# Kernel tuning notes

Measured on AMD Instinct MI355X. Metric: run time of the kernel, lower is better.

Reference implementation:

```python
import jax, jax.numpy as jnp
import numpy as np

N_ITER = 5  # from init_kwargs


def setup_inputs() -> dict:
    key = jax.random.key(0)
    k1, k2 = jax.random.split(key)
    K, F, B = 4, 513, 4000
    Xr = jax.random.normal(k1, (K, F, B), dtype=jnp.float32)
    Xi = jax.random.normal(k2, (K, F, B), dtype=jnp.float32)
    return {"Xr": Xr, "Xi": Xi}


def _auxiva(X):
    # X: complex64 (K, F, B)
    K, F, B = X.shape
    # XXh[i,j,f,b] = X[i,f,b] * conj(X[j,f,b])
    XXh = jnp.einsum('ifb,jfb->ijfb', X, X.conj())
    Wh = jnp.tile(jnp.eye(K, dtype=X.dtype)[None], (F, 1, 1))  # (F, K, K)
    for _ in range(N_ITER):
        Y = jnp.einsum('fsc,cfb->sfb', Wh, X)          # demix: (K, F, B)
        r = jnp.linalg.norm(Y, axis=1)                  # (K, B), real
        phi = 1.0 / (2.0 * r)                           # laplace contrast
        # V[k,i,j,f] = mean_b phi[k,b] * XXh[i,j,f,b]  (avoid (K,K,K,F,B) blowup)
        V = jnp.einsum('kb,ijfb->kijf', phi.astype(X.dtype), XXh) / B
        for k in range(K):                              # sequential IP updates
            M = jnp.einsum('fik,kjf->fij', Wh, V[k])    # (F, K, K)
            w = jnp.linalg.inv(M)[:, :, k].conj()       # (F, K)
            denom = jnp.sqrt(jnp.einsum('fc,ckf,fk->f', w, V[k], w.conj()))
            Wh = Wh.at[:, k, :].set(w / denom[:, None])
    Y = jnp.einsum('fsc,cfb->sfb', Wh, X)
    scale = jnp.linalg.inv(Wh)[:, :, 0]                 # projection back: (F, K)
    return jnp.einsum('sfb,fs->sfb', Y, scale)


def reference(Xr, Xi):
    X = (Xr + 1j * Xi).astype(jnp.complex64)
    return _auxiva(X)
```

## Files before the change

kernel.cpp:

```cpp
#include <hip/hip_runtime.h>
#include <hip/hip_bf16.h>
#include <math.h>

#define K 4
#define F 513
#define B 4000
#define NIT 5
#define FB (F*B)
#define KB (K*B)
#define DFC 4
#define NDF 129
#define NBC 8
#define BCH (B/NBC)

__device__ float2 g_Wh[F*16];
__device__ float2 g_Vp[NBC*64*F];
__device__ float2 g_scale[F*4];
__device__ float  g_r2p[NDF*KB];
__device__ float4 g_phiT[B];

struct cd { double re, im; };
__device__ inline cd mkcd(double r, double i){ cd z; z.re=r; z.im=i; return z; }
__device__ inline cd cmul(cd a, cd b){ return mkcd(a.re*b.re - a.im*b.im, a.re*b.im + a.im*b.re); }
__device__ inline cd cadd(cd a, cd b){ return mkcd(a.re+b.re, a.im+b.im); }
__device__ inline cd csub(cd a, cd b){ return mkcd(a.re-b.re, a.im-b.im); }
__device__ inline cd conj_(cd a){ return mkcd(a.re, -a.im); }
__device__ inline cd cdiv(cd a, cd b){
  double d = b.re*b.re + b.im*b.im;
  return mkcd((a.re*b.re + a.im*b.im)/d, (a.im*b.re - a.re*b.im)/d);
}

__device__ inline void invcol4(const cd M[4][4], int kk, cd x[4]){
  int r0 = (kk==0)?1:0;
  int r1 = (kk<=1)?2:1;
  int r2 = (kk<=2)?3:2;
  cd cof[4];
  #pragma unroll
  for (int i=0;i<4;++i){
    int c0 = (i==0)?1:0;
    int c1 = (i<=1)?2:1;
    int c2 = (i<=2)?3:2;
    cd m = cadd(csub(cmul(M[r0][c0], csub(cmul(M[r1][c1],M[r2][c2]), cmul(M[r1][c2],M[r2][c1]))),
                     cmul(M[r0][c1], csub(cmul(M[r1][c0],M[r2][c2]), cmul(M[r1][c2],M[r2][c0])))),
                cmul(M[r0][c2], csub(cmul(M[r1][c0],M[r2][c1]), cmul(M[r1][c1],M[r2][c0]))));
    if ((kk+i)&1) m = mkcd(-m.re,-m.im);
    cof[i] = m;
  }
  cd det = mkcd(0.0,0.0);
  #pragma unroll
  for (int i=0;i<4;++i) det = cadd(det, cmul(M[kk][i], cof[i]));
  cd idet = cdiv(mkcd(1.0,0.0), det);
  #pragma unroll
  for (int i=0;i<4;++i) x[i] = cmul(cof[i], idet);
}


__global__ void init_kernel(){
  int t = blockIdx.x*blockDim.x + threadIdx.x;
  if (t < F*16){
    int sc = t & 15; int s = sc >> 2, c = sc & 3;
    g_Wh[t] = make_float2(s==c ? 1.0f : 0.0f, 0.0f);
  }
}

__global__ __launch_bounds__(256) void demix_part_kernel(
    const float* __restrict__ Xr, const float* __restrict__ Xi){
  int t = blockIdx.x*blockDim.x + threadIdx.x;
  if (t >= B/2) return;
  int b = 2*t;
  int y = blockIdx.y;
  int f0 = y*DFC, f1 = min(f0+DFC, F);
  float acc0[K], acc1[K];
  #pragma unroll
  for (int s=0;s<K;++s){ acc0[s]=0.0f; acc1[s]=0.0f; }
  for (int f=f0; f<f1; ++f){
    float2 xr[K], xi[K];
    #pragma unroll
    for (int c=0;c<K;++c){
      int idx = c*FB + f*B + b;
      xr[c] = *reinterpret_cast<const float2*>(Xr + idx);
      xi[c] = *reinterpret_cast<const float2*>(Xi + idx);
    }
    const float2* w = g_Wh + f*16;
    #pragma unroll
    for (int s=0;s<K;++s){
      float yr0=0.0f, yi0=0.0f, yr1=0.0f, yi1=0.0f;
      #pragma unroll
      for (int c=0;c<K;++c){
        float2 ww = w[s*4+c];
        yr0 += ww.x*xr[c].x - ww.y*xi[c].x;
        yi0 += ww.x*xi[c].x + ww.y*xr[c].x;
        yr1 += ww.x*xr[c].y - ww.y*xi[c].y;
        yi1 += ww.x*xi[c].y + ww.y*xr[c].y;
      }
      acc0[s] += yr0*yr0 + yi0*yi0;
      acc1[s] += yr1*yr1 + yi1*yi1;
    }
  }
  #pragma unroll
  for (int s=0;s<K;++s)
    *reinterpret_cast<float2*>(g_r2p + y*KB + s*B + b) = make_float2(acc0[s], acc1[s]);
}

__global__ __launch_bounds__(256) void phi_kernel(){
  int b = blockIdx.x*blockDim.x + threadIdx.x;
  if (b >= B) return;
  int k = blockIdx.y;
  float s = 0.0f;
  #pragma unroll 8
  for (int y=0; y<NDF; ++y) s += g_r2p[y*KB + k*B + b];
  reinterpret_cast<float*>(g_phiT)[b*4 + k] = 0.5f / sqrtf(s);
}

__global__ __launch_bounds__(256, 4) void v_kernel(
    const float* __restrict__ Xr, const float* __restrict__ Xi){
  int f = blockIdx.x;
  int y = blockIdx.y;
  int tid = threadIdx.x;
  float acc[64];
  #pragma unroll
  for (int q=0;q<64;++q) acc[q]=0.0f;

  if (tid < BCH/2){
    int b = y*BCH + 2*tid;
    float4 ph0 = g_phiT[b];
    float4 ph1 = g_phiT[b+1];
    float pk0[K] = {ph0.x, ph0.y, ph0.z, ph0.w};
    float pk1[K] = {ph1.x, ph1.y, ph1.z, ph1.w};
    float2 xr[K], xi[K];
    #pragma unroll
    for (int c=0;c<K;++c){
      int idx = c*FB + f*B + b;
      xr[c] = *reinterpret_cast<const float2*>(Xr + idx);
      xi[c] = *reinterpret_cast<const float2*>(Xi + idx);
    }
    {
      float p[16];
      #pragma unroll
      for (int i=0;i<4;++i) p[i] = xr[i].x*xr[i].x + xi[i].x*xi[i].x;
      int s = 4;
      #pragma unroll
      for (int i=0;i<4;++i){
        #pragma unroll
        for (int j=i+1;j<4;++j){
          p[s++] = xr[i].x*xr[j].x + xi[i].x*xi[j].x;
          p[s++] = xi[i].x*xr[j].x - xr[i].x*xi[j].x;
        }
      }
      #pragma unroll
      for (int k=0;k<K;++k){
        #pragma unroll
        for (int q=0;q<16;++q) acc[k*16+q] += pk0[k]*p[q];
      }
    }
    {
      float p[16];
      #pragma unroll
      for (int i=0;i<4;++i) p[i] = xr[i].y*xr[i].y + xi[i].y*xi[i].y;
      int s = 4;
      #pragma unroll
      for (int i=0;i<4;++i){
        #pragma unroll
        for (int j=i+1;j<4;++j){
          p[s++] = xr[i].y*xr[j].y + xi[i].y*xi[j].y;
          p[s++] = xi[i].y*xr[j].y - xr[i].y*xi[j].y;
        }
      }
      #pragma unroll
      for (int k=0;k<K;++k){
        #pragma unroll
        for (int q=0;q<16;++q) acc[k*16+q] += pk1[k]*p[q];
      }
    }
  }

  int lane = tid & 63, wave = tid >> 6;
  #pragma unroll
  for (int d=0; d<6; ++d){
    const int sh = 1<<d;
    const bool hi = (lane & sh) != 0;
    #pragma unroll
    for (int m=0; m<(32>>d); ++m){
      float keep = hi ? acc[2*m+1] : acc[2*m];
      float send = hi ? acc[2*m]   : acc[2*m+1];
      acc[m] = keep + __shfl_xor(send, sh);
    }
  }

  __shared__ float part[4*64];
  __shared__ float red[64];
  part[wave*64 + lane] = acc[0];
  __syncthreads();
  if (tid < 64){
    red[tid] = (part[tid] + part[64+tid] + part[128+tid] + part[192+tid]) * (1.0f/B);
  }
  __syncthreads();
  if (tid < 64){
    int k = tid >> 4, ij = tid & 15, i = ij >> 2, j = ij & 3;
    float re, im;
    if (i == j){ re = red[k*16 + i]; im = 0.0f; }
    else {
      int a = min(i,j), c2 = max(i,j);
      int pidx = (a==0) ? (c2-1) : ((a==1) ? (c2+1) : 5);
      re = red[k*16 + 4 + 2*pidx];
      im = red[k*16 + 5 + 2*pidx];
      if (i > j) im = -im;
    }
    g_Vp[(y*64 + (unsigned)tid)*F + f] = make_float2(re, im);
  }
}

__global__ __launch_bounds__(64) void update_kernel(int do_scale){
  int f = blockIdx.x*blockDim.x + threadIdx.x;
  if (f >= F) return;
  cd W[4][4];
  #pragma unroll
  for (int s=0;s<4;++s)
    #pragma unroll
    for (int c=0;c<4;++c){ float2 w = g_Wh[f*16+s*4+c]; W[s][c] = mkcd((double)w.x,(double)w.y); }

  #pragma unroll
  for (int k=0;k<4;++k){
    cd Vk[4][4];
    #pragma unroll
    for (int i=0;i<4;++i)
      #pragma unroll
      for (int j=0;j<4;++j){
        float2 vv = make_float2(0.0f, 0.0f);
        #pragma unroll
        for (int y=0;y<NBC;++y){
          float2 t2 = g_Vp[(y*64 + (k*4+i)*4 + j)*F + f];
          vv.x += t2.x; vv.y += t2.y;
        }
        Vk[i][j] = mkcd((double)vv.x,(double)vv.y);
      }
    cd M[4][4];
    #pragma unroll
    for (int i=0;i<4;++i)
      #pragma unroll
      for (int j=0;j<4;++j){
        cd s = mkcd(0.0,0.0);
        #pragma unroll
        for (int c=0;c<4;++c) s = cadd(s, cmul(W[i][c], Vk[c][j]));
        M[i][j] = s;
      }
    cd x[4];
    invcol4(M, k, x);
    cd w[4];
    #pragma unroll
    for (int c=0;c<4;++c) w[c] = conj_(x[c]);
    double dre = 0.0;
    #pragma unroll
    for (int j=0;j<4;++j){
      cd tj = mkcd(0.0,0.0);
      #pragma unroll
      for (int c=0;c<4;++c) tj = cadd(tj, cmul(w[c], Vk[c][j]));
      dre += tj.re*w[j].re + tj.im*w[j].im;
    }
    double inv_denom = rsqrt(dre > 0.0 ? dre : 1e-300);
    #pragma unroll
    for (int c=0;c<4;++c) W[k][c] = mkcd(w[c].re*inv_denom, w[c].im*inv_denom);
  }
  #pragma unroll
  for (int s=0;s<4;++s)
    #pragma unroll
    for (int c=0;c<4;++c) g_Wh[f*16+s*4+c] = make_float2((float)W[s][c].re, (float)W[s][c].im);

  if (do_scale){
    cd x[4];
    invcol4(W, 0, x);
    #pragma unroll
    for (int s=0;s<4;++s) g_scale[f*4+s] = make_float2((float)x[s].re, (float)x[s].im);
  }
}

__global__ __launch_bounds__(256) void final_kernel(
    const float* __restrict__ Xr, const float* __restrict__ Xi,
    __hip_bfloat162* __restrict__ out){
  int t = blockIdx.x*blockDim.x + threadIdx.x;
  if (t >= B/2) return;
  int b = 2*t;
  int f0 = blockIdx.y*DFC, f1 = min(f0+DFC, F);
  for (int f=f0; f<f1; ++f){
    float2 xr[K], xi[K];
    #pragma unroll
    for (int c=0;c<K;++c){
      int idx = c*FB + f*B + b;
      xr[c] = *reinterpret_cast<const float2*>(Xr + idx);
      xi[c] = *reinterpret_cast<const float2*>(Xi + idx);
    }
    const float2* w = g_Wh + f*16;
    #pragma unroll
    for (int s=0;s<K;++s){
      float yr0=0.0f, yi0=0.0f, yr1=0.0f, yi1=0.0f;
      #pragma unroll
      for (int c=0;c<K;++c){
        float2 ww = w[s*4+c];
        yr0 += ww.x*xr[c].x - ww.y*xi[c].x;
        yi0 += ww.x*xi[c].x + ww.y*xr[c].x;
        yr1 += ww.x*xr[c].y - ww.y*xi[c].y;
        yi1 += ww.x*xi[c].y + ww.y*xr[c].y;
      }
      float2 sc = g_scale[f*4+s];
      union { __hip_bfloat162 h2[2]; uint2 u; } uu;
      uu.h2[0].x = __float2bfloat16(yr0*sc.x - yi0*sc.y);
      uu.h2[0].y = __float2bfloat16(yr0*sc.y + yi0*sc.x);
      uu.h2[1].x = __float2bfloat16(yr1*sc.x - yi1*sc.y);
      uu.h2[1].y = __float2bfloat16(yr1*sc.y + yi1*sc.x);
      *reinterpret_cast<uint2*>(out + s*FB + f*B + b) = uu.u;
    }
  }
}

extern "C" void kernel_launch(void* const* d_in, const int* in_sizes, int n_in,
                              void* d_out, int out_size, void* d_ws, size_t ws_size,
                              hipStream_t stream){
  const float* Xr = (const float*)d_in[1];
  const float* Xi = (const float*)d_in[0];
  __hip_bfloat162* out = (__hip_bfloat162*)d_out;

  init_kernel<<<33, 256, 0, stream>>>();
  dim3 gD((B/2 + 255)/256, NDF);
  dim3 gP((B + 255)/256, K);
  dim3 gV(F, NBC);
  for (int it=0; it<NIT; ++it){
    demix_part_kernel<<<gD, 256, 0, stream>>>(Xr, Xi);
    phi_kernel<<<gP, 256, 0, stream>>>();
    v_kernel<<<gV, 256, 0, stream>>>(Xr, Xi);
    update_kernel<<<(F + 63)/64, 64, 0, stream>>>(it == NIT-1 ? 1 : 0);
  }
  final_kernel<<<gD, 256, 0, stream>>>(Xr, Xi, out);
}
```

Measured before the change: 411.3 us.

## Reduce V partials with atomics, drop init kernel, specialize first iteration

The init kernel is removed, and the first iteration's demix and update use the identity Wh directly. V partials are now accumulated with atomicAdd into a single 64xF buffer that phi_kernel zeroes, so update_kernel no longer sums eight partial buffers. v_kernel processes four samples per thread with half as many B chunks and a lower occupancy hint. The frequency loops are unrolled with a separate tail for the last frequency. Atomics add contention and make the reduction order nondeterministic.

```diff
diff --git a/kernel.cpp b/kernel.cpp
--- a/kernel.cpp
+++ b/kernel.cpp
@@ -10,11 +10,11 @@
 #define KB (K*B)
 #define DFC 4
 #define NDF 129
-#define NBC 8
+#define NBC 4
 #define BCH (B/NBC)
 
 __device__ float2 g_Wh[F*16];
-__device__ float2 g_Vp[NBC*64*F];
+__device__ float2 g_V[64*F];
 __device__ float2 g_scale[F*4];
 __device__ float  g_r2p[NDF*KB];
 __device__ float4 g_phiT[B];
@@ -55,25 +55,17 @@
 }
 
 
-__global__ void init_kernel(){
-  int t = blockIdx.x*blockDim.x + threadIdx.x;
-  if (t < F*16){
-    int sc = t & 15; int s = sc >> 2, c = sc & 3;
-    g_Wh[t] = make_float2(s==c ? 1.0f : 0.0f, 0.0f);
-  }
-}
-
 __global__ __launch_bounds__(256) void demix_part_kernel(
-    const float* __restrict__ Xr, const float* __restrict__ Xi){
+    const float* __restrict__ Xr, const float* __restrict__ Xi, int it0){
   int t = blockIdx.x*blockDim.x + threadIdx.x;
   if (t >= B/2) return;
   int b = 2*t;
   int y = blockIdx.y;
-  int f0 = y*DFC, f1 = min(f0+DFC, F);
   float acc0[K], acc1[K];
   #pragma unroll
   for (int s=0;s<K;++s){ acc0[s]=0.0f; acc1[s]=0.0f; }
-  for (int f=f0; f<f1; ++f){
+
+  auto body = [&](int f){
     float2 xr[K], xi[K];
     #pragma unroll
     for (int c=0;c<K;++c){
@@ -81,21 +73,37 @@
       xr[c] = *reinterpret_cast<const float2*>(Xr + idx);
       xi[c] = *reinterpret_cast<const float2*>(Xi + idx);
     }
-    const float2* w = g_Wh + f*16;
-    #pragma unroll
-    for (int s=0;s<K;++s){
-      float yr0=0.0f, yi0=0.0f, yr1=0.0f, yi1=0.0f;
-      #pragma unroll
-      for (int c=0;c<K;++c){
-        float2 ww = w[s*4+c];
-        yr0 += ww.x*xr[c].x - ww.y*xi[c].x;
-        yi0 += ww.x*xi[c].x + ww.y*xr[c].x;
-        yr1 += ww.x*xr[c].y - ww.y*xi[c].y;
-        yi1 += ww.x*xi[c].y + ww.y*xr[c].y;
-      }
-      acc0[s] += yr0*yr0 + yi0*yi0;
-      acc1[s] += yr1*yr1 + yi1*yi1;
-    }
+    if (it0){
+      #pragma unroll
+      for (int s=0;s<K;++s){
+        acc0[s] += xr[s].x*xr[s].x + xi[s].x*xi[s].x;
+        acc1[s] += xr[s].y*xr[s].y + xi[s].y*xi[s].y;
+      }
+    } else {
+      const float2* w = g_Wh + f*16;
+      #pragma unroll
+      for (int s=0;s<K;++s){
+        float yr0=0.0f, yi0=0.0f, yr1=0.0f, yi1=0.0f;
+        #pragma unroll
+        for (int c=0;c<K;++c){
+          float2 ww = w[s*4+c];
+          yr0 += ww.x*xr[c].x - ww.y*xi[c].x;
+          yi0 += ww.x*xi[c].x + ww.y*xr[c].x;
+          yr1 += ww.x*xr[c].y - ww.y*xi[c].y;
+          yi1 += ww.x*xi[c].y + ww.y*xr[c].y;
+        }
+        acc0[s] += yr0*yr0 + yi0*yi0;
+        acc1[s] += yr1*yr1 + yi1*yi1;
+      }
+    }
+  };
+
+  if (y < 128){
+    int f0 = y*DFC;
+    #pragma unroll
+    for (int ff=0; ff<DFC; ++ff) body(f0+ff);
+  } else {
+    body(512);
   }
   #pragma unroll
   for (int s=0;s<K;++s)
@@ -104,15 +112,18 @@
 
 __global__ __launch_bounds__(256) void phi_kernel(){
   int b = blockIdx.x*blockDim.x + threadIdx.x;
+  int k = blockIdx.y;
+  int g = (blockIdx.y*gridDim.x + blockIdx.x)*256 + threadIdx.x;
+  float* vz = reinterpret_cast<float*>(g_V);
+  for (int j=g; j<64*F*2; j+=16384) vz[j] = 0.0f;
   if (b >= B) return;
-  int k = blockIdx.y;
   float s = 0.0f;
   #pragma unroll 8
   for (int y=0; y<NDF; ++y) s += g_r2p[y*KB + k*B + b];
   reinterpret_cast<float*>(g_phiT)[b*4 + k] = 0.5f / sqrtf(s);
 }
 
-__global__ __launch_bounds__(256, 4) void v_kernel(
+__global__ __launch_bounds__(256, 3) void v_kernel(
     const float* __restrict__ Xr, const float* __restrict__ Xi){
   int f = blockIdx.x;
   int y = blockIdx.y;
@@ -121,55 +132,46 @@
   #pragma unroll
   for (int q=0;q<64;++q) acc[q]=0.0f;
 
-  if (tid < BCH/2){
-    int b = y*BCH + 2*tid;
-    float4 ph0 = g_phiT[b];
-    float4 ph1 = g_phiT[b+1];
-    float pk0[K] = {ph0.x, ph0.y, ph0.z, ph0.w};
-    float pk1[K] = {ph1.x, ph1.y, ph1.z, ph1.w};
-    float2 xr[K], xi[K];
+  if (tid < BCH/4){
+    int b = y*BCH + 4*tid;
+    float4 ph[4];
+    #pragma unroll
+    for (int u=0;u<4;++u) ph[u] = g_phiT[b+u];
+    float2 xr[K][2], xi[K][2];
     #pragma unroll
     for (int c=0;c<K;++c){
       int idx = c*FB + f*B + b;
-      xr[c] = *reinterpret_cast<const float2*>(Xr + idx);
-      xi[c] = *reinterpret_cast<const float2*>(Xi + idx);
-    }
-    {
+      xr[c][0] = *reinterpret_cast<const float2*>(Xr + idx);
+      xr[c][1] = *reinterpret_cast<const float2*>(Xr + idx + 2);
+      xi[c][0] = *reinterpret_cast<const float2*>(Xi + idx);
+      xi[c][1] = *reinterpret_cast<const float2*>(Xi + idx + 2);
+    }
+    #pragma unroll
+    for (int u=0;u<4;++u){
+      const int h = u >> 1;
+      float vr[K], vi[K], pk[K];
+      #pragma unroll
+      for (int c=0;c<K;++c){
+        vr[c] = (u&1) ? xr[c][h].y : xr[c][h].x;
+        vi[c] = (u&1) ? xi[c][h].y : xi[c][h].x;
+      }
+      pk[0]=ph[u].x; pk[1]=ph[u].y; pk[2]=ph[u].z; pk[3]=ph[u].w;
       float p[16];
       #pragma unroll
-      for (int i=0;i<4;++i) p[i] = xr[i].x*xr[i].x + xi[i].x*xi[i].x;
+      for (int i=0;i<4;++i) p[i] = vr[i]*vr[i] + vi[i]*vi[i];
       int s = 4;
       #pragma unroll
       for (int i=0;i<4;++i){
         #pragma unroll
         for (int j=i+1;j<4;++j){
-          p[s++] = xr[i].x*xr[j].x + xi[i].x*xi[j].x;
-          p[s++] = xi[i].x*xr[j].x - xr[i].x*xi[j].x;
+          p[s++] = vr[i]*vr[j] + vi[i]*vi[j];
+          p[s++] = vi[i]*vr[j] - vr[i]*vi[j];
         }
       }
       #pragma unroll
       for (int k=0;k<K;++k){
         #pragma unroll
-        for (int q=0;q<16;++q) acc[k*16+q] += pk0[k]*p[q];
-      }
-    }
-    {
-      float p[16];
-      #pragma unroll
-      for (int i=0;i<4;++i) p[i] = xr[i].y*xr[i].y + xi[i].y*xi[i].y;
-      int s = 4;
-      #pragma unroll
-      for (int i=0;i<4;++i){
-        #pragma unroll
-        for (int j=i+1;j<4;++j){
-          p[s++] = xr[i].y*xr[j].y + xi[i].y*xi[j].y;
-          p[s++] = xi[i].y*xr[j].y - xr[i].y*xi[j].y;
-        }
-      }
-      #pragma unroll
-      for (int k=0;k<K;++k){
-        #pragma unroll
-        for (int q=0;q<16;++q) acc[k*16+q] += pk1[k]*p[q];
+        for (int q=0;q<16;++q) acc[k*16+q] += pk[k]*p[q];
       }
     }
   }
@@ -206,18 +208,32 @@
       im = red[k*16 + 5 + 2*pidx];
       if (i > j) im = -im;
     }
-    g_Vp[(y*64 + (unsigned)tid)*F + f] = make_float2(re, im);
-  }
-}
-
-__global__ __launch_bounds__(64) void update_kernel(int do_scale){
+    float* dst = reinterpret_cast<float*>(g_V) + ((unsigned)tid*F + f)*2;
+    atomicAdd(dst,   re);
+    atomicAdd(dst+1, im);
+  }
+}
+
+__global__ __launch_bounds__(64, 1) void update_kernel(int it0, int do_scale){
   int f = blockIdx.x*blockDim.x + threadIdx.x;
   if (f >= F) return;
+
+  float2 Vf[64];
+  #pragma unroll
+  for (int q=0;q<64;++q) Vf[q] = g_V[q*F + f];
+
   cd W[4][4];
-  #pragma unroll
-  for (int s=0;s<4;++s)
-    #pragma unroll
-    for (int c=0;c<4;++c){ float2 w = g_Wh[f*16+s*4+c]; W[s][c] = mkcd((double)w.x,(double)w.y); }
+  if (it0){
+    #pragma unroll
+    for (int s=0;s<4;++s)
+      #pragma unroll
+      for (int c=0;c<4;++c) W[s][c] = mkcd(s==c ? 1.0 : 0.0, 0.0);
+  } else {
+    #pragma unroll
+    for (int s=0;s<4;++s)
+      #pragma unroll
+      for (int c=0;c<4;++c){ float2 w = g_Wh[f*16+s*4+c]; W[s][c] = mkcd((double)w.x,(double)w.y); }
+  }
 
   #pragma unroll
   for (int k=0;k<4;++k){
@@ -226,12 +242,7 @@
     for (int i=0;i<4;++i)
       #pragma unroll
       for (int j=0;j<4;++j){
-        float2 vv = make_float2(0.0f, 0.0f);
-        #pragma unroll
-        for (int y=0;y<NBC;++y){
-          float2 t2 = g_Vp[(y*64 + (k*4+i)*4 + j)*F + f];
-          vv.x += t2.x; vv.y += t2.y;
-        }
+        float2 vv = Vf[(k*4+i)*4+j];
         Vk[i][j] = mkcd((double)vv.x,(double)vv.y);
       }
     cd M[4][4];
@@ -280,8 +291,9 @@
   int t = blockIdx.x*blockDim.x + threadIdx.x;
   if (t >= B/2) return;
   int b = 2*t;
-  int f0 = blockIdx.y*DFC, f1 = min(f0+DFC, F);
-  for (int f=f0; f<f1; ++f){
+  int y = blockIdx.y;
+
+  auto body = [&](int f){
     float2 xr[K], xi[K];
     #pragma unroll
     for (int c=0;c<K;++c){
@@ -309,6 +321,14 @@
       uu.h2[1].y = __float2bfloat16(yr1*sc.y + yi1*sc.x);
       *reinterpret_cast<uint2*>(out + s*FB + f*B + b) = uu.u;
     }
+  };
+
+  if (y < 128){
+    int f0 = y*DFC;
+    #pragma unroll
+    for (int ff=0; ff<DFC; ++ff) body(f0+ff);
+  } else {
+    body(512);
   }
 }
 
@@ -319,15 +339,14 @@
   const float* Xi = (const float*)d_in[0];
   __hip_bfloat162* out = (__hip_bfloat162*)d_out;
 
-  init_kernel<<<33, 256, 0, stream>>>();
   dim3 gD((B/2 + 255)/256, NDF);
   dim3 gP((B + 255)/256, K);
   dim3 gV(F, NBC);
   for (int it=0; it<NIT; ++it){
-    demix_part_kernel<<<gD, 256, 0, stream>>>(Xr, Xi);
+    demix_part_kernel<<<gD, 256, 0, stream>>>(Xr, Xi, it == 0 ? 1 : 0);
     phi_kernel<<<gP, 256, 0, stream>>>();
     v_kernel<<<gV, 256, 0, stream>>>(Xr, Xi);
-    update_kernel<<<(F + 63)/64, 64, 0, stream>>>(it == NIT-1 ? 1 : 0);
+    update_kernel<<<(F + 63)/64, 64, 0, stream>>>(it == 0 ? 1 : 0, it == NIT-1 ? 1 : 0);
   }
   final_kernel<<<gD, 256, 0, stream>>>(Xr, Xi, out);
 }
```

After: 381.0 us. -7.4%, faster.
